# Performance work log

Hardware: AMD Instinct MI355X
Metric: run time of the kernel (lower is better)

## Reference

```python
import jax, jax.numpy as jnp
import numpy as np
import math

DIM = 384
HEADS = 6
HEAD_DIM = DIM // HEADS
MLP_HIDDEN = int(DIM * 2.0)


def layer_norm(x, g, b, eps=1e-5):
    mu = jnp.mean(x, axis=-1, keepdims=True)
    var = jnp.mean((x - mu) ** 2, axis=-1, keepdims=True)
    return (x - mu) * jax.lax.rsqrt(var + eps) * g + b


def setup_inputs() -> dict:
    key = jax.random.key(0)
    ks = jax.random.split(key, 12)
    B, N = 4, 2048
    s = 0.02
    return {
        "x": jax.random.normal(ks[0], (B, N, DIM), dtype=jnp.float32),
        "pos": jax.random.normal(ks[1], (B, N, 3), dtype=jnp.float32),
        "qkv_w": jax.random.normal(ks[2], (DIM, 3 * DIM), dtype=jnp.float32) * s,
        "qkv_b": jnp.zeros((3 * DIM,), jnp.float32),
        "proj_w": jax.random.normal(ks[3], (DIM, DIM), dtype=jnp.float32) * s,
        "proj_b": jnp.zeros((DIM,), jnp.float32),
        "mlp_w1": jax.random.normal(ks[4], (DIM, MLP_HIDDEN), dtype=jnp.float32) * s,
        "mlp_b1": jnp.zeros((MLP_HIDDEN,), jnp.float32),
        "mlp_w2": jax.random.normal(ks[5], (MLP_HIDDEN, DIM), dtype=jnp.float32) * s,
        "mlp_b2": jnp.zeros((DIM,), jnp.float32),
        "ln1_g": jnp.ones((DIM,), jnp.float32),
        "ln1_b": jnp.zeros((DIM,), jnp.float32),
        "ln2_g": jnp.ones((DIM,), jnp.float32),
        "ln2_b": jnp.zeros((DIM,), jnp.float32),
    }


def reference(x, pos, qkv_w, qkv_b, proj_w, proj_b, mlp_w1, mlp_b1,
              mlp_w2, mlp_b2, ln1_g, ln1_b, ln2_g, ln2_b):
    B, N, D = x.shape
    H, Hd = HEADS, HEAD_DIM
    # qkv projection
    qkv = layer_norm(x, ln1_g, ln1_b) @ qkv_w + qkv_b          # [B,N,3D]
    qkv = qkv.reshape(B, N, 3, H, Hd)
    q = jnp.transpose(qkv[:, :, 0], (0, 2, 1, 3))               # [B,H,N,Hd]
    k = jnp.transpose(qkv[:, :, 1], (0, 2, 1, 3))
    v = jnp.transpose(qkv[:, :, 2], (0, 2, 1, 3))
    # pairwise squared-distance bias: exp(-||p_i - p_j||^2)
    rel = pos[:, :, None, :] - pos[:, None, :, :]               # [B,N,N,3]
    dist = jnp.exp(-jnp.sum(rel ** 2, axis=-1))                 # [B,N,N]
    scale = 1.0 / math.sqrt(Hd)
    attn = jnp.einsum('bhqd,bhkd->bhqk', q, k) * scale + dist[:, None, :, :]
    attn = jax.nn.softmax(attn, axis=-1)
    out = jnp.einsum('bhqk,bhkd->bhqd', attn, v)                # [B,H,N,Hd]
    out = jnp.transpose(out, (0, 2, 1, 3)).reshape(B, N, D)
    out = out @ proj_w + proj_b
    x = x + out
    h = layer_norm(x, ln2_g, ln2_b)
    h = jax.nn.gelu(h @ mlp_w1 + mlp_b1, approximate=False) @ mlp_w2 + mlp_b2
    return x + h
```

## Files before the change

### kernel.cpp

```cpp
#include <hip/hip_runtime.h>
#include <hip/hip_bf16.h>
#include <math.h>

#define DIMD 384
#define NHEADS 6
#define HD 64
#define MLPH 768
#define SEQ 2048
#define NBATCH 4
#define NTOK (NBATCH*SEQ)

typedef __hip_bfloat16 bf16;

typedef __attribute__((ext_vector_type(8))) short bf16x8;
typedef __attribute__((ext_vector_type(4))) float f32x4;

#define LOG2E 1.44269504088896340736f

static __device__ inline float fexp2(float x) { return __builtin_amdgcn_exp2f(x); }

static __device__ inline f32x4 mfma16(bf16x8 a, bf16x8 b, f32x4 c) {
    return __builtin_amdgcn_mfma_f32_16x16x32_bf16(a, b, c, 0, 0, 0);
}

static __device__ inline unsigned int cvtpk(float lo, float hi) {
    unsigned int r;
    asm("v_cvt_pk_bf16_f32 %0, %1, %2" : "=v"(r) : "v"(lo), "v"(hi));
    return r;
}
static __device__ inline float bflo(unsigned int u) { return __builtin_bit_cast(float, u << 16); }
static __device__ inline float bfhi(unsigned int u) { return __builtin_bit_cast(float, u & 0xffff0000u); }

static __device__ inline void gld16(const void* g, void* l) {
    __builtin_amdgcn_global_load_lds(
        (const __attribute__((address_space(1))) unsigned int*)g,
        (__attribute__((address_space(3))) unsigned int*)l, 16, 0, 0);
}

__global__ __launch_bounds__(256) void ln_k(const float* __restrict__ x,
                                            const float* __restrict__ gm,
                                            const float* __restrict__ bt,
                                            bf16* __restrict__ out) {
    int row = blockIdx.x * 4 + (threadIdx.x >> 6);
    int l = threadIdx.x & 63;
    const float* xr = x + (size_t)row * DIMD;
    float v[6];
#pragma unroll
    for (int j = 0; j < 6; ++j) v[j] = xr[l + 64 * j];
    float s = 0.f, s2 = 0.f;
#pragma unroll
    for (int j = 0; j < 6; ++j) { s += v[j]; s2 += v[j] * v[j]; }
#pragma unroll
    for (int m = 1; m < 64; m <<= 1) { s += __shfl_xor(s, m); s2 += __shfl_xor(s2, m); }
    float mu = s * (1.f / DIMD);
    float var = s2 * (1.f / DIMD) - mu * mu;
    float rs = rsqrtf(var + 1e-5f);
    bf16* orow = out + (size_t)row * DIMD;
#pragma unroll
    for (int j = 0; j < 6; ++j) {
        int i = l + 64 * j;
        orow[i] = __float2bfloat16((v[j] - mu) * rs * gm[i] + bt[i]);
    }
}

__global__ __launch_bounds__(256) void wtrans_k(const float* __restrict__ W,
                                                bf16* __restrict__ WT,
                                                int K, int N) {
    __shared__ float t[32][33];
    int tx = threadIdx.x & 31, ty = threadIdx.x >> 5;
    int nb = blockIdx.x * 32, kb = blockIdx.y * 32;
#pragma unroll
    for (int i = 0; i < 4; ++i)
        t[ty + 8 * i][tx] = W[(size_t)(kb + ty + 8 * i) * N + nb + tx];
    __syncthreads();
#pragma unroll
    for (int i = 0; i < 4; ++i)
        WT[(size_t)(nb + ty + 8 * i) * K + kb + tx] = __float2bfloat16(t[tx][ty + 8 * i]);
}

__global__ __launch_bounds__(256) void vtrans_k(const bf16* __restrict__ v_,
                                                bf16* __restrict__ vT_) {
    const unsigned short* v = (const unsigned short*)v_;
    unsigned short* vT = (unsigned short*)vT_;
    __shared__ unsigned short t[32][33];
    int tx = threadIdx.x & 31, ty = threadIdx.x >> 5;
    int nb = blockIdx.x * 32, db = blockIdx.y * 32;
    int bh = blockIdx.z;
    const unsigned short* src = v + (size_t)bh * SEQ * HD;
#pragma unroll
    for (int i = 0; i < 4; ++i)
        t[ty + 8 * i][tx] = src[(size_t)(nb + ty + 8 * i) * HD + db + tx];
    __syncthreads();
    unsigned short* dst = vT + (size_t)bh * HD * SEQ;
#pragma unroll
    for (int i = 0; i < 4; ++i)
        dst[(size_t)(db + ty + 8 * i) * SEQ + nb + tx] = t[tx][ty + 8 * i];
}

__global__ __launch_bounds__(256) void dist_k(const float* __restrict__ pos,
                                              bf16* __restrict__ DP) {
    int blk = blockIdx.x;
    int w = blk & 3, qt = (blk >> 2) & 31, b = blk >> 7;
    int l = threadIdx.x & 63, tt = threadIdx.x >> 6;
    int lq = l & 15, g = l >> 4;
    int q = qt * 64 + w * 16 + lq;
    const float* pq = pos + ((size_t)b * SEQ + q) * 3;
    float px = pq[0], py = pq[1], pz = pq[2];
    const float* posb = pos + (size_t)b * SEQ * 3;
    char* base = (char*)DP + (size_t)blk * 65536;
    for (int j = 0; j < 8; ++j) {
        int t = tt * 8 + j;
#pragma unroll
        for (int m = 0; m < 2; ++m) {
            int k0 = t * 64 + 32 * m + 4 * g;
            float a[24];
            const float* pk = posb + 3 * k0;
            *(f32x4*)&a[0]  = *(const f32x4*)pk;
            *(f32x4*)&a[4]  = *(const f32x4*)(pk + 4);
            *(f32x4*)&a[8]  = *(const f32x4*)(pk + 8);
            const float* pk2 = posb + 3 * (k0 + 16);
            *(f32x4*)&a[12] = *(const f32x4*)pk2;
            *(f32x4*)&a[16] = *(const f32x4*)(pk2 + 4);
            *(f32x4*)&a[20] = *(const f32x4*)(pk2 + 8);
            float o8[8];
#pragma unroll
            for (int r = 0; r < 8; ++r) {
                float dx = px - a[3 * r], dy = py - a[3 * r + 1], dz = pz - a[3 * r + 2];
                o8[r] = fexp2(-LOG2E * (dx * dx + dy * dy + dz * dz)) * LOG2E;
            }
            uint4 o;
            o.x = cvtpk(o8[0], o8[1]); o.y = cvtpk(o8[2], o8[3]);
            o.z = cvtpk(o8[4], o8[5]); o.w = cvtpk(o8[6], o8[7]);
            *(uint4*)(base + ((size_t)t * 2 + m) * 1024 + l * 16) = o;
        }
    }
}

template <int EPI>
__global__ __launch_bounds__(256) void gemm_k(const bf16* __restrict__ A,
                                              const bf16* __restrict__ WT,
                                              const float* __restrict__ bias,
                                              const float* __restrict__ resid,
                                              float* __restrict__ outf,
                                              bf16* __restrict__ ob0,
                                              bf16* __restrict__ ob1,
                                              bf16* __restrict__ ob2,
                                              int K, int Nw) {
    __shared__ __align__(16) char Als[2][8192];
    __shared__ __align__(16) char Bls[2][8192];
    int tid = threadIdx.x;
    int w = tid >> 6, l = tid & 63;
    int c = l & 15, g = l >> 4;
    int m0 = blockIdx.y * 64, n0 = blockIdx.x * 64;
    const char* Ag = (const char*)A + (size_t)m0 * K * 2;
    const char* Bg = (const char*)WT + (size_t)n0 * K * 2;
    int K2 = K * 2;

    f32x4 acc[4];
#pragma unroll
    for (int nt = 0; nt < 4; ++nt) acc[nt] = (f32x4){0.f, 0.f, 0.f, 0.f};

    auto stage = [&](int t, int bi) {
#pragma unroll
        for (int p = 0; p < 2; ++p) {
            int chunk = p * 256 + tid;
            int r = chunk >> 3;
            int cc = ((chunk & 7) ^ (r & 7)) << 4;
            gld16(Ag + (size_t)r * K2 + t * 128 + cc, &Als[bi][chunk * 16]);
            gld16(Bg + (size_t)r * K2 + t * 128 + cc, &Bls[bi][chunk * 16]);
        }
    };

    stage(0, 0);
    int kcn = K >> 6;
    int arow = (16 * w + c) * 128;
    int sw = c & 7;
    for (int t = 0; t < kcn; ++t) {
        int bi = t & 1;
        __syncthreads();
        if (t + 1 < kcn) stage(t + 1, bi ^ 1);
#pragma unroll
        for (int kk = 0; kk < 2; ++kk) {
            int ch = ((kk * 4 + g) ^ sw) << 4;
            bf16x8 af;
            __builtin_memcpy(&af, &Als[bi][arow + ch], 16);
#pragma unroll
            for (int nt = 0; nt < 4; ++nt) {
                bf16x8 bfr;
                __builtin_memcpy(&bfr, &Bls[bi][(nt * 16 + c) * 128 + ch], 16);
                acc[nt] = mfma16(af, bfr, acc[nt]);
            }
        }
    }

#pragma unroll
    for (int nt = 0; nt < 4; ++nt) {
        int ntb = n0 + nt * 16;
#pragma unroll
        for (int r = 0; r < 4; ++r) {
            int m = m0 + 16 * w + 4 * g + r;
            int n = ntb + c;
            float val = acc[nt][r] + bias[n];
            if (EPI == 0) {
                int which = ntb / DIMD;
                int rem = ntb - which * DIMD;
                int h = rem >> 6;
                int d = (rem & 63) + c;
                int b = m >> 11, s = m & (SEQ - 1);
                bf16* dp = which == 0 ? ob0 : (which == 1 ? ob1 : ob2);
                dp[(((size_t)b * NHEADS + h) * SEQ + s) * HD + d] = __float2bfloat16(val);
            } else if (EPI == 1 || EPI == 3) {
                val += resid[(size_t)m * Nw + n];
                outf[(size_t)m * Nw + n] = val;
            } else {
                float ge = 0.5f * val * (1.0f + erff(val * 0.70710678118654752f));
                ob0[(size_t)m * Nw + n] = __float2bfloat16(ge);
            }
        }
    }
}

__global__ __launch_bounds__(256) void attn_k(const bf16* __restrict__ q,
                                              const bf16* __restrict__ k,
                                              const bf16* __restrict__ vT,
                                              const bf16* __restrict__ DP,
                                              bf16* __restrict__ out) {
    __shared__ __align__(16) char Kls[2][8192];
    __shared__ __align__(16) char Vls[2][8192];
    __shared__ __align__(16) unsigned int P_lds[4][16][20];

    int tid = threadIdx.x;
    int w = tid >> 6, l = tid & 63;
    int lq = l & 15, g = l >> 4;
    int qt = blockIdx.x & 31;
    int bh = blockIdx.x >> 5;
    int b = bh / NHEADS, h = bh % NHEADS;
    int qrow = qt * 64 + w * 16 + lq;

    const bf16* qp = q + ((size_t)bh * SEQ + qrow) * HD + 8 * g;
    bf16x8 qf0 = *(const bf16x8*)qp;
    bf16x8 qf1 = *(const bf16x8*)(qp + 32);

    const char* kgb = (const char*)(k + (size_t)bh * SEQ * HD);
    const char* vgb = (const char*)(vT + (size_t)bh * HD * SEQ);
    const char* dpb = (const char*)DP + ((size_t)((b * 32 + qt) * 4 + w)) * 65536 + l * 16;

    const float SC2 = 0.125f * LOG2E;
    float lrun = 0.f;
    f32x4 oacc[4];
#pragma unroll
    for (int dt = 0; dt < 4; ++dt) oacc[dt] = (f32x4){0.f, 0.f, 0.f, 0.f};

    auto stage = [&](int t, int bi) {
#pragma unroll
        for (int p = 0; p < 2; ++p) {
            int chunk = p * 256 + tid;
            int r = chunk >> 3, c = chunk & 7;
            int cc = (c ^ (r & 7)) << 4;
            gld16(kgb + (size_t)t * 8192 + r * 128 + cc, &Kls[bi][chunk * 16]);
            gld16(vgb + (size_t)r * 4096 + t * 128 + cc, &Vls[bi][chunk * 16]);
        }
    };

    stage(0, 0);
    uint4 cdp0 = *(const uint4*)(dpb);
    uint4 cdp1 = *(const uint4*)(dpb + 1024);

    int swq = lq & 7;
    for (int t = 0; t < 32; ++t) {
        int bi = t & 1;
        __syncthreads();
        uint4 ndp0 = {0, 0, 0, 0}, ndp1 = {0, 0, 0, 0};
        if (t + 1 < 32) {
            stage(t + 1, bi ^ 1);
            const char* dpn = dpb + (size_t)(t + 1) * 2048;
            ndp0 = *(const uint4*)(dpn);
            ndp1 = *(const uint4*)(dpn + 1024);
        }

        f32x4 st[4];
#pragma unroll
        for (int s = 0; s < 4; ++s) {
            int ro = (16 * s + lq) * 128;
            bf16x8 klo, khi;
            __builtin_memcpy(&klo, &Kls[bi][ro + ((g ^ swq) << 4)], 16);
            __builtin_memcpy(&khi, &Kls[bi][ro + (((4 + g) ^ swq) << 4)], 16);
            f32x4 z = (f32x4){0.f, 0.f, 0.f, 0.f};
            st[s] = mfma16(klo, qf0, z);
            st[s] = mfma16(khi, qf1, st[s]);
        }

#pragma unroll
        for (int m = 0; m < 2; ++m) {
            uint4 cd = m == 0 ? cdp0 : cdp1;
            f32x4 s0v = st[2 * m], s1v = st[2 * m + 1];
            float p[8];
            p[0] = fexp2(s0v[0] * SC2 + bflo(cd.x));
            p[1] = fexp2(s0v[1] * SC2 + bfhi(cd.x));
            p[2] = fexp2(s0v[2] * SC2 + bflo(cd.y));
            p[3] = fexp2(s0v[3] * SC2 + bfhi(cd.y));
            p[4] = fexp2(s1v[0] * SC2 + bflo(cd.z));
            p[5] = fexp2(s1v[1] * SC2 + bfhi(cd.z));
            p[6] = fexp2(s1v[2] * SC2 + bflo(cd.w));
            p[7] = fexp2(s1v[3] * SC2 + bfhi(cd.w));
            float ps = 0.f;
#pragma unroll
            for (int i = 0; i < 8; ++i) ps += p[i];
            ps += __shfl_xor(ps, 16);
            ps += __shfl_xor(ps, 32);
            lrun += ps;

            P_lds[w][lq][2 * g] = cvtpk(p[0], p[1]);
            P_lds[w][lq][2 * g + 1] = cvtpk(p[2], p[3]);
            P_lds[w][lq][8 + 2 * g] = cvtpk(p[4], p[5]);
            P_lds[w][lq][8 + 2 * g + 1] = cvtpk(p[6], p[7]);
            bf16x8 pf;
            __builtin_memcpy(&pf, &P_lds[w][lq][4 * g], 16);

#pragma unroll
            for (int dt = 0; dt < 4; ++dt) {
                int rv = (16 * dt + lq) * 128;
                bf16x8 vf;
                __builtin_memcpy(&vf, &Vls[bi][rv + (((4 * m + g) ^ swq) << 4)], 16);
                oacc[dt] = mfma16(vf, pf, oacc[dt]);
            }
        }
        cdp0 = ndp0; cdp1 = ndp1;
    }

    float inv = 1.f / lrun;
    bf16* op = out + ((size_t)b * SEQ + qrow) * DIMD + h * HD + 4 * g;
#pragma unroll
    for (int dt = 0; dt < 4; ++dt) {
        unsigned int t2[2];
        t2[0] = cvtpk(oacc[dt][0] * inv, oacc[dt][1] * inv);
        t2[1] = cvtpk(oacc[dt][2] * inv, oacc[dt][3] * inv);
        __builtin_memcpy(op + dt * 16, t2, 8);
    }
}

extern "C" void kernel_launch(void* const* d_in, const int* in_sizes, int n_in,
                              void* d_out, int out_size, void* d_ws, size_t ws_size,
                              hipStream_t stream) {
    const float* x      = (const float*)d_in[0];
    const float* pos    = (const float*)d_in[1];
    const float* qkv_w  = (const float*)d_in[2];
    const float* qkv_b  = (const float*)d_in[3];
    const float* proj_w = (const float*)d_in[4];
    const float* proj_b = (const float*)d_in[5];
    const float* mlp_w1 = (const float*)d_in[6];
    const float* mlp_b1 = (const float*)d_in[7];
    const float* mlp_w2 = (const float*)d_in[8];
    const float* mlp_b2 = (const float*)d_in[9];
    const float* ln1_g  = (const float*)d_in[10];
    const float* ln1_b  = (const float*)d_in[11];
    const float* ln2_g  = (const float*)d_in[12];
    const float* ln2_b  = (const float*)d_in[13];

    char* p = (char*)d_ws;
    size_t off = 0;
    auto alloc = [&](size_t bytes) {
        char* r = p + off;
        off = (off + bytes + 255) & ~(size_t)255;
        return r;
    };
    bf16* WT1 = (bf16*)alloc((size_t)1152 * 384 * 2);
    bf16* WT2 = (bf16*)alloc((size_t)384 * 384 * 2);
    bf16* WT3 = (bf16*)alloc((size_t)384 * 768 * 2);
    bf16* WT4 = (bf16*)alloc((size_t)768 * 384 * 2);
    bf16* xn  = (bf16*)alloc((size_t)NTOK * DIMD * 2);
    bf16* xn2 = (bf16*)alloc((size_t)NTOK * DIMD * 2);
    bf16* qb  = (bf16*)alloc((size_t)NTOK * DIMD * 2);
    bf16* kb  = (bf16*)alloc((size_t)NTOK * DIMD * 2);
    bf16* vb  = (bf16*)alloc((size_t)NTOK * DIMD * 2);
    bf16* vTb = (bf16*)alloc((size_t)NTOK * DIMD * 2);
    bf16* ao  = (bf16*)alloc((size_t)NTOK * DIMD * 2);
    float* x1 = (float*)alloc((size_t)NTOK * DIMD * 4);
    bf16* hh  = (bf16*)alloc((size_t)NTOK * MLPH * 2);
    bf16* dtab = (bf16*)alloc((size_t)NBATCH * SEQ * SEQ * 2);
    if (off > ws_size) return;

    wtrans_k<<<dim3(36, 12), 256, 0, stream>>>(qkv_w, WT1, 384, 1152);
    wtrans_k<<<dim3(12, 12), 256, 0, stream>>>(proj_w, WT2, 384, 384);
    wtrans_k<<<dim3(24, 12), 256, 0, stream>>>(mlp_w1, WT3, 384, 768);
    wtrans_k<<<dim3(12, 24), 256, 0, stream>>>(mlp_w2, WT4, 768, 384);

    dist_k<<<NBATCH * 32 * 4, 256, 0, stream>>>(pos, dtab);

    ln_k<<<NTOK / 4, 256, 0, stream>>>(x, ln1_g, ln1_b, xn);
    gemm_k<0><<<dim3(1152 / 64, NTOK / 64), 256, 0, stream>>>(
        xn, WT1, qkv_b, nullptr, nullptr, qb, kb, vb, 384, 1152);
    vtrans_k<<<dim3(SEQ / 32, HD / 32, NBATCH * NHEADS), 256, 0, stream>>>(vb, vTb);
    attn_k<<<NBATCH * NHEADS * (SEQ / 64), 256, 0, stream>>>(qb, kb, vTb, dtab, ao);
    gemm_k<1><<<dim3(384 / 64, NTOK / 64), 256, 0, stream>>>(
        ao, WT2, proj_b, x, x1, nullptr, nullptr, nullptr, 384, 384);
    ln_k<<<NTOK / 4, 256, 0, stream>>>(x1, ln2_g, ln2_b, xn2);
    gemm_k<2><<<dim3(768 / 64, NTOK / 64), 256, 0, stream>>>(
        xn2, WT3, mlp_b1, nullptr, nullptr, hh, nullptr, nullptr, 384, 768);
    gemm_k<3><<<dim3(384 / 64, NTOK / 64), 256, 0, stream>>>(
        hh, WT4, mlp_b2, x1, (float*)d_out, nullptr, nullptr, nullptr, 768, 384);
}
```

Before: 154.1 us.

## Use 128x128 register-tiled GEMM for QKV and MLP-up; defer softmax sum reduction

Adds a gemm128_k kernel in which each of four waves computes a 64x64 sub-tile (4x4 MFMA accumulators) of a 128x128 block. It replaces the 64x64 GEMM for the QKV projection and the first MLP layer, which raises operand reuse from LDS and cuts global loads per FLOP. The cost is more registers and fewer blocks per launch. Separately, the attention kernel now keeps the row-sum per lane and does the cross-lane shuffle reduction once after the key loop instead of on every tile.

```diff
diff --git a/kernel.cpp b/kernel.cpp
--- a/kernel.cpp
+++ b/kernel.cpp
@@ -137,14 +137,98 @@
 }
 
 template <int EPI>
+__global__ __launch_bounds__(256) void gemm128_k(const bf16* __restrict__ A,
+                                                 const bf16* __restrict__ WT,
+                                                 const float* __restrict__ bias,
+                                                 bf16* __restrict__ ob0,
+                                                 bf16* __restrict__ ob1,
+                                                 bf16* __restrict__ ob2,
+                                                 int K, int Nw) {
+    __shared__ __align__(16) char Als[2][8192];
+    __shared__ __align__(16) char Bls[2][8192];
+    int tid = threadIdx.x;
+    int w = tid >> 6, l = tid & 63;
+    int c = l & 15, g = l >> 4;
+    int wr = w >> 1, wc = w & 1;
+    int m0 = blockIdx.y * 128, n0 = blockIdx.x * 128;
+    const char* Ag = (const char*)A + (size_t)m0 * K * 2;
+    const char* Bg = (const char*)WT + (size_t)n0 * K * 2;
+    int K2 = K * 2;
+
+    f32x4 acc[4][4];
+#pragma unroll
+    for (int mi = 0; mi < 4; ++mi)
+#pragma unroll
+        for (int ni = 0; ni < 4; ++ni) acc[mi][ni] = (f32x4){0.f, 0.f, 0.f, 0.f};
+
+    auto stage = [&](int t, int bi) {
+#pragma unroll
+        for (int p = 0; p < 2; ++p) {
+            int chunk = p * 256 + tid;
+            int r = chunk >> 2;
+            int cc = ((chunk & 3) ^ (r & 3)) << 4;
+            gld16(Ag + (size_t)r * K2 + t * 64 + cc, &Als[bi][chunk * 16]);
+            gld16(Bg + (size_t)r * K2 + t * 64 + cc, &Bls[bi][chunk * 16]);
+        }
+    };
+
+    stage(0, 0);
+    int kcn = K >> 5;
+    for (int t = 0; t < kcn; ++t) {
+        int bi = t & 1;
+        __syncthreads();
+        if (t + 1 < kcn) stage(t + 1, bi ^ 1);
+        bf16x8 af[4], bfr[4];
+#pragma unroll
+        for (int mi = 0; mi < 4; ++mi) {
+            int row = wr * 64 + mi * 16 + c;
+            __builtin_memcpy(&af[mi], &Als[bi][row * 64 + ((g ^ (row & 3)) << 4)], 16);
+        }
+#pragma unroll
+        for (int ni = 0; ni < 4; ++ni) {
+            int row = wc * 64 + ni * 16 + c;
+            __builtin_memcpy(&bfr[ni], &Bls[bi][row * 64 + ((g ^ (row & 3)) << 4)], 16);
+        }
+#pragma unroll
+        for (int mi = 0; mi < 4; ++mi)
+#pragma unroll
+            for (int ni = 0; ni < 4; ++ni)
+                acc[mi][ni] = mfma16(af[mi], bfr[ni], acc[mi][ni]);
+    }
+
+#pragma unroll
+    for (int mi = 0; mi < 4; ++mi) {
+#pragma unroll
+        for (int ni = 0; ni < 4; ++ni) {
+            int ntb = n0 + wc * 64 + ni * 16;
+#pragma unroll
+            for (int r = 0; r < 4; ++r) {
+                int m = m0 + wr * 64 + mi * 16 + 4 * g + r;
+                int n = ntb + c;
+                float val = acc[mi][ni][r] + bias[n];
+                if (EPI == 0) {
+                    int which = ntb / DIMD;
+                    int rem = ntb - which * DIMD;
+                    int h = rem >> 6;
+                    int d = (rem & 63) + c;
+                    int b = m >> 11, s = m & (SEQ - 1);
+                    bf16* dp = which == 0 ? ob0 : (which == 1 ? ob1 : ob2);
+                    dp[(((size_t)b * NHEADS + h) * SEQ + s) * HD + d] = __float2bfloat16(val);
+                } else {
+                    float ge = 0.5f * val * (1.0f + erff(val * 0.70710678118654752f));
+                    ob0[(size_t)m * Nw + n] = __float2bfloat16(ge);
+                }
+            }
+        }
+    }
+}
+
+template <int EPI>
 __global__ __launch_bounds__(256) void gemm_k(const bf16* __restrict__ A,
                                               const bf16* __restrict__ WT,
                                               const float* __restrict__ bias,
                                               const float* __restrict__ resid,
                                               float* __restrict__ outf,
-                                              bf16* __restrict__ ob0,
-                                              bf16* __restrict__ ob1,
-                                              bf16* __restrict__ ob2,
                                               int K, int Nw) {
     __shared__ __align__(16) char Als[2][8192];
     __shared__ __align__(16) char Bls[2][8192];
@@ -201,21 +285,8 @@
             int m = m0 + 16 * w + 4 * g + r;
             int n = ntb + c;
             float val = acc[nt][r] + bias[n];
-            if (EPI == 0) {
-                int which = ntb / DIMD;
-                int rem = ntb - which * DIMD;
-                int h = rem >> 6;
-                int d = (rem & 63) + c;
-                int b = m >> 11, s = m & (SEQ - 1);
-                bf16* dp = which == 0 ? ob0 : (which == 1 ? ob1 : ob2);
-                dp[(((size_t)b * NHEADS + h) * SEQ + s) * HD + d] = __float2bfloat16(val);
-            } else if (EPI == 1 || EPI == 3) {
-                val += resid[(size_t)m * Nw + n];
-                outf[(size_t)m * Nw + n] = val;
-            } else {
-                float ge = 0.5f * val * (1.0f + erff(val * 0.70710678118654752f));
-                ob0[(size_t)m * Nw + n] = __float2bfloat16(ge);
-            }
+            val += resid[(size_t)m * Nw + n];
+            outf[(size_t)m * Nw + n] = val;
         }
     }
 }
@@ -246,7 +317,7 @@
     const char* dpb = (const char*)DP + ((size_t)((b * 32 + qt) * 4 + w)) * 65536 + l * 16;
 
     const float SC2 = 0.125f * LOG2E;
-    float lrun = 0.f;
+    float lloc = 0.f;
     f32x4 oacc[4];
 #pragma unroll
     for (int dt = 0; dt < 4; ++dt) oacc[dt] = (f32x4){0.f, 0.f, 0.f, 0.f};
@@ -303,12 +374,8 @@
             p[5] = fexp2(s1v[1] * SC2 + bfhi(cd.z));
             p[6] = fexp2(s1v[2] * SC2 + bflo(cd.w));
             p[7] = fexp2(s1v[3] * SC2 + bfhi(cd.w));
-            float ps = 0.f;
-#pragma unroll
-            for (int i = 0; i < 8; ++i) ps += p[i];
-            ps += __shfl_xor(ps, 16);
-            ps += __shfl_xor(ps, 32);
-            lrun += ps;
+#pragma unroll
+            for (int i = 0; i < 8; ++i) lloc += p[i];
 
             P_lds[w][lq][2 * g] = cvtpk(p[0], p[1]);
             P_lds[w][lq][2 * g + 1] = cvtpk(p[2], p[3]);
@@ -328,6 +395,9 @@
         cdp0 = ndp0; cdp1 = ndp1;
     }
 
+    float lrun = lloc;
+    lrun += __shfl_xor(lrun, 16);
+    lrun += __shfl_xor(lrun, 32);
     float inv = 1.f / lrun;
     bf16* op = out + ((size_t)b * SEQ + qrow) * DIMD + h * HD + 4 * g;
 #pragma unroll
@@ -388,15 +458,15 @@
     dist_k<<<NBATCH * 32 * 4, 256, 0, stream>>>(pos, dtab);
 
     ln_k<<<NTOK / 4, 256, 0, stream>>>(x, ln1_g, ln1_b, xn);
-    gemm_k<0><<<dim3(1152 / 64, NTOK / 64), 256, 0, stream>>>(
-        xn, WT1, qkv_b, nullptr, nullptr, qb, kb, vb, 384, 1152);
+    gemm128_k<0><<<dim3(1152 / 128, NTOK / 128), 256, 0, stream>>>(
+        xn, WT1, qkv_b, qb, kb, vb, 384, 1152);
     vtrans_k<<<dim3(SEQ / 32, HD / 32, NBATCH * NHEADS), 256, 0, stream>>>(vb, vTb);
     attn_k<<<NBATCH * NHEADS * (SEQ / 64), 256, 0, stream>>>(qb, kb, vTb, dtab, ao);
     gemm_k<1><<<dim3(384 / 64, NTOK / 64), 256, 0, stream>>>(
-        ao, WT2, proj_b, x, x1, nullptr, nullptr, nullptr, 384, 384);
+        ao, WT2, proj_b, x, x1, 384, 384);
     ln_k<<<NTOK / 4, 256, 0, stream>>>(x1, ln2_g, ln2_b, xn2);
-    gemm_k<2><<<dim3(768 / 64, NTOK / 64), 256, 0, stream>>>(
-        xn2, WT3, mlp_b1, nullptr, nullptr, hh, nullptr, nullptr, 384, 768);
+    gemm128_k<2><<<dim3(768 / 128, NTOK / 128), 256, 0, stream>>>(
+        xn2, WT3, mlp_b1, hh, nullptr, nullptr, 384, 768);
     gemm_k<3><<<dim3(384 / 64, NTOK / 64), 256, 0, stream>>>(
-        hh, WT4, mlp_b2, x1, (float*)d_out, nullptr, nullptr, nullptr, 768, 384);
-}
+        hh, WT4, mlp_b2, x1, (float*)d_out, 768, 384);
+}
```

After: 152.9 us. Within noise of the previous version (-0.8%).
